# Optimization experiments

Measured on AMD Instinct MI355X. Metric: run time of the kernel, lower is better.

The kernel has to match this reference:

```python
import jax, jax.numpy as jnp
import numpy as np

B, N, F_IN, F_HID, F_OUT = 64, 1024, 64, 128, 64

def setup_inputs() -> dict:
    key = jax.random.key(0)
    ks = jax.random.split(key, 6)
    x = jax.random.normal(ks[0], (B, N, F_IN), dtype=jnp.float32)
    adj = jax.random.uniform(ks[1], (B, N, N), dtype=jnp.float32)
    mask = jax.random.randint(ks[2], (B, N), 0, 2).astype(bool)
    W1 = jax.random.normal(ks[3], (F_IN, F_HID), dtype=jnp.float32) * (1.0 / np.sqrt(F_IN))
    b1 = jnp.zeros((F_HID,), dtype=jnp.float32)
    W2 = jax.random.normal(ks[4], (F_HID, F_OUT), dtype=jnp.float32) * (1.0 / np.sqrt(F_HID))
    b2 = jnp.zeros((F_OUT,), dtype=jnp.float32)
    eps = jnp.zeros((1,), dtype=jnp.float32)
    return {"x": x, "adj": adj, "mask": mask, "W1": W1, "b1": b1, "W2": W2, "b2": b2, "eps": eps}

def reference(x, adj, mask, W1, b1, W2, b2, eps):
    # neighbor aggregation: out[b,i,f] = sum_j adj[b,i,j] * x[b,j,f]
    agg = jnp.einsum('bij,bjf->bif', adj, x)
    # add_loop=True: (1 + eps) * x + aggregated neighbors
    h = (1.0 + eps[0]) * x + agg
    # 2-layer GIN MLP applied per node (only valid nodes contribute in the
    # torch version via gather/scatter; invalid positions are zeroed)
    h = jax.nn.relu(h @ W1 + b1) @ W2 + b2
    return jnp.where(mask[..., None], h, jnp.zeros((), dtype=h.dtype))
```

## Files before the change

kernel.cpp:

```cpp
#include <hip/hip_runtime.h>


#define N_    1024
#define FIN   64
#define FHID  128
#define FOUT  64
#define JT    64
#define AS_LD 68
#define H1_LD 132

__global__ __launch_bounds__(256) void gin_fused(
    const float* __restrict__ x, const float* __restrict__ adj,
    const int* __restrict__ mask, const float* __restrict__ W1,
    const float* __restrict__ b1, const float* __restrict__ W2,
    const float* __restrict__ b2, const float* __restrict__ epsp,
    float* __restrict__ out)
{
    __shared__ float region1[8448];
    __shared__ float hs[64 * 64];

    float* xs  = region1;
    float* as_ = region1 + 4096;
    float* h1s = region1;

    const int t  = threadIdx.x;
    const int b  = blockIdx.x >> 4;
    const int i0 = (blockIdx.x & 15) * 64;

    const int fi = (t & 15) * 4;
    const int ri = (t >> 4) * 4;

    const float* xb   = x   + (size_t)b * N_ * FIN;
    const float* adjb = adj + (size_t)b * N_ * N_ + (size_t)i0 * N_;

    float4 acc[4];
    #pragma unroll
    for (int ii = 0; ii < 4; ++ii) acc[ii] = make_float4(0.f, 0.f, 0.f, 0.f);

    for (int jc = 0; jc < N_ / JT; ++jc) {
        const int j0 = jc * JT;

        const float4* xsrc = reinterpret_cast<const float4*>(xb + j0 * FIN);
        #pragma unroll
        for (int k = 0; k < 4; ++k) {
            const int l = t + 256 * k;
            reinterpret_cast<float4*>(xs)[l] = xsrc[l];
        }
        #pragma unroll
        for (int k = 0; k < 4; ++k) {
            const int l  = t + 256 * k;
            const int r  = l >> 4;
            const int c4 = (l & 15) * 4;
            const float4 v = *reinterpret_cast<const float4*>(adjb + (size_t)r * N_ + j0 + c4);
            *reinterpret_cast<float4*>(&as_[r * AS_LD + c4]) = v;
        }
        __syncthreads();

        #pragma unroll 4
        for (int jj = 0; jj < JT; ++jj) {
            const float4 xv = *reinterpret_cast<const float4*>(&xs[jj * FIN + fi]);
            const float a0 = as_[(ri + 0) * AS_LD + jj];
            const float a1 = as_[(ri + 1) * AS_LD + jj];
            const float a2 = as_[(ri + 2) * AS_LD + jj];
            const float a3 = as_[(ri + 3) * AS_LD + jj];
            acc[0].x += a0 * xv.x; acc[0].y += a0 * xv.y; acc[0].z += a0 * xv.z; acc[0].w += a0 * xv.w;
            acc[1].x += a1 * xv.x; acc[1].y += a1 * xv.y; acc[1].z += a1 * xv.z; acc[1].w += a1 * xv.w;
            acc[2].x += a2 * xv.x; acc[2].y += a2 * xv.y; acc[2].z += a2 * xv.z; acc[2].w += a2 * xv.w;
            acc[3].x += a3 * xv.x; acc[3].y += a3 * xv.y; acc[3].z += a3 * xv.z; acc[3].w += a3 * xv.w;
        }
        __syncthreads();
    }

    const float se = 1.0f + epsp[0];
    #pragma unroll
    for (int ii = 0; ii < 4; ++ii) {
        const float4 xv = *reinterpret_cast<const float4*>(xb + (size_t)(i0 + ri + ii) * FIN + fi);
        float4 h;
        h.x = acc[ii].x + se * xv.x;
        h.y = acc[ii].y + se * xv.y;
        h.z = acc[ii].z + se * xv.z;
        h.w = acc[ii].w + se * xv.w;
        *reinterpret_cast<float4*>(&hs[(ri + ii) * FIN + fi]) = h;
    }
    __syncthreads();

    {
        const int k4 = (t & 31) * 4;
        const int rb = (t >> 5) * 8;
        float4 hacc[8];
        const float4 b1v = *reinterpret_cast<const float4*>(b1 + k4);
        #pragma unroll
        for (int r = 0; r < 8; ++r) hacc[r] = b1v;

        #pragma unroll 4
        for (int j = 0; j < FIN; ++j) {
            const float4 w1v = *reinterpret_cast<const float4*>(W1 + j * FHID + k4);
            #pragma unroll
            for (int r = 0; r < 8; ++r) {
                const float hv = hs[(rb + r) * FIN + j];
                hacc[r].x += hv * w1v.x; hacc[r].y += hv * w1v.y;
                hacc[r].z += hv * w1v.z; hacc[r].w += hv * w1v.w;
            }
        }
        #pragma unroll
        for (int r = 0; r < 8; ++r) {
            float4 v;
            v.x = fmaxf(hacc[r].x, 0.f); v.y = fmaxf(hacc[r].y, 0.f);
            v.z = fmaxf(hacc[r].z, 0.f); v.w = fmaxf(hacc[r].w, 0.f);
            *reinterpret_cast<float4*>(&h1s[(rb + r) * H1_LD + k4]) = v;
        }
    }
    __syncthreads();

    {
        float4 oacc[4];
        const float4 b2v = *reinterpret_cast<const float4*>(b2 + fi);
        #pragma unroll
        for (int ii = 0; ii < 4; ++ii) oacc[ii] = b2v;

        #pragma unroll 4
        for (int j = 0; j < FHID; ++j) {
            const float4 w2v = *reinterpret_cast<const float4*>(W2 + j * FOUT + fi);
            #pragma unroll
            for (int ii = 0; ii < 4; ++ii) {
                const float hv = h1s[(ri + ii) * H1_LD + j];
                oacc[ii].x += hv * w2v.x; oacc[ii].y += hv * w2v.y;
                oacc[ii].z += hv * w2v.z; oacc[ii].w += hv * w2v.w;
            }
        }
        #pragma unroll
        for (int ii = 0; ii < 4; ++ii) {
            const int gi = i0 + ri + ii;
            const int m  = mask[b * N_ + gi];
            float4 o = oacc[ii];
            if (!m) o = make_float4(0.f, 0.f, 0.f, 0.f);
            *reinterpret_cast<float4*>(out + ((size_t)b * N_ + gi) * FOUT + fi) = o;
        }
    }
}

extern "C" void kernel_launch(void* const* d_in, const int* in_sizes, int n_in,
                              void* d_out, int out_size, void* d_ws, size_t ws_size,
                              hipStream_t stream) {
    const float* x    = (const float*)d_in[0];
    const float* adj  = (const float*)d_in[1];
    const int*   mask = (const int*)  d_in[2];
    const float* W1   = (const float*)d_in[3];
    const float* b1   = (const float*)d_in[4];
    const float* W2   = (const float*)d_in[5];
    const float* b2   = (const float*)d_in[6];
    const float* eps  = (const float*)d_in[7];
    float* out = (float*)d_out;

    dim3 grid(64 * 16);
    dim3 block(256);
    gin_fused<<<grid, block, 0, stream>>>(x, adj, mask, W1, b1, W2, b2, eps, out);
}
```

Before: 465.4 us.

## Use bf16 MFMA for adjacency aggregation with transposed bf16 LDS tiles

Replaces the scalar FP32 FMA loop for the adj·x aggregation with 32x32x16 bf16 MFMA instructions. Each 64x64 tile of adj and x is converted to bf16 on load and stored in LDS, with x transposed so both operands are K-contiguous. This targets the FP32 ALU-bound inner loop and halves LDS footprint. The cost is lower precision from rounding adj and x (1024-term sums) to bf16, plus extra conversion work and strided scalar loads of x.

```diff
diff --git a/kernel.cpp b/kernel.cpp
--- a/kernel.cpp
+++ b/kernel.cpp
@@ -5,9 +5,18 @@
 #define FIN   64
 #define FHID  128
 #define FOUT  64
-#define JT    64
-#define AS_LD 68
+#define HS_LD 68
 #define H1_LD 132
+#define FROW  9
+
+typedef __attribute__((ext_vector_type(16))) float f32x16;
+typedef __attribute__((ext_vector_type(8)))  short s16x8;
+
+__device__ inline short f2bf(float f) {
+    union { float f; unsigned int u; } v; v.f = f;
+    unsigned int r = v.u + 0x7fffu + ((v.u >> 16) & 1u);
+    return (short)(r >> 16);
+}
 
 __global__ __launch_bounds__(256) void gin_fused(
     const float* __restrict__ x, const float* __restrict__ adj,
@@ -16,71 +25,83 @@
     const float* __restrict__ b2, const float* __restrict__ epsp,
     float* __restrict__ out)
 {
-    __shared__ float region1[8448];
-    __shared__ float hs[64 * 64];
+    __shared__ s16x8 region1[2112];
+    __shared__ float hs[64 * HS_LD];
 
-    float* xs  = region1;
-    float* as_ = region1 + 4096;
-    float* h1s = region1;
+    s16x8 (*asf)[FROW] = reinterpret_cast<s16x8 (*)[FROW]>(region1);
+    s16x8 (*xtf)[FROW] = reinterpret_cast<s16x8 (*)[FROW]>(region1 + 576);
+    float* h1s = reinterpret_cast<float*>(region1);
 
-    const int t  = threadIdx.x;
-    const int b  = blockIdx.x >> 4;
-    const int i0 = (blockIdx.x & 15) * 64;
-
-    const int fi = (t & 15) * 4;
-    const int ri = (t >> 4) * 4;
+    const int t    = threadIdx.x;
+    const int lane = t & 63;
+    const int w    = t >> 6;
+    const int b    = blockIdx.x >> 4;
+    const int i0   = (blockIdx.x & 15) * 64;
 
     const float* xb   = x   + (size_t)b * N_ * FIN;
     const float* adjb = adj + (size_t)b * N_ * N_ + (size_t)i0 * N_;
 
-    float4 acc[4];
+    const int l31  = lane & 31;
+    const int half = lane >> 5;
+    const int mrow = (w & 1) * 32;
+    const int ncol = (w >> 1) * 32;
+
+    const int sr = t >> 2;
+    const int sc = (t & 3) * 16;
+    const int sg = (t & 3) * 2;
+
+    f32x16 acc;
     #pragma unroll
-    for (int ii = 0; ii < 4; ++ii) acc[ii] = make_float4(0.f, 0.f, 0.f, 0.f);
+    for (int r = 0; r < 16; ++r) acc[r] = 0.f;
 
-    for (int jc = 0; jc < N_ / JT; ++jc) {
-        const int j0 = jc * JT;
+    for (int jc = 0; jc < N_ / 64; ++jc) {
+        const int j0 = jc * 64;
 
-        const float4* xsrc = reinterpret_cast<const float4*>(xb + j0 * FIN);
-        #pragma unroll
-        for (int k = 0; k < 4; ++k) {
-            const int l = t + 256 * k;
-            reinterpret_cast<float4*>(xs)[l] = xsrc[l];
+        {
+            const float* ar = adjb + (size_t)sr * N_ + j0 + sc;
+            const float4 p0 = *reinterpret_cast<const float4*>(ar);
+            const float4 p1 = *reinterpret_cast<const float4*>(ar + 4);
+            const float4 p2 = *reinterpret_cast<const float4*>(ar + 8);
+            const float4 p3 = *reinterpret_cast<const float4*>(ar + 12);
+            s16x8 f0, f1;
+            f0[0] = f2bf(p0.x); f0[1] = f2bf(p0.y); f0[2] = f2bf(p0.z); f0[3] = f2bf(p0.w);
+            f0[4] = f2bf(p1.x); f0[5] = f2bf(p1.y); f0[6] = f2bf(p1.z); f0[7] = f2bf(p1.w);
+            f1[0] = f2bf(p2.x); f1[1] = f2bf(p2.y); f1[2] = f2bf(p2.z); f1[3] = f2bf(p2.w);
+            f1[4] = f2bf(p3.x); f1[5] = f2bf(p3.y); f1[6] = f2bf(p3.z); f1[7] = f2bf(p3.w);
+            asf[sr][sg]     = f0;
+            asf[sr][sg + 1] = f1;
         }
-        #pragma unroll
-        for (int k = 0; k < 4; ++k) {
-            const int l  = t + 256 * k;
-            const int r  = l >> 4;
-            const int c4 = (l & 15) * 4;
-            const float4 v = *reinterpret_cast<const float4*>(adjb + (size_t)r * N_ + j0 + c4);
-            *reinterpret_cast<float4*>(&as_[r * AS_LD + c4]) = v;
+        {
+            s16x8 q0, q1;
+            #pragma unroll
+            for (int jj = 0; jj < 8; ++jj)
+                q0[jj] = f2bf(xb[(size_t)(j0 + w * 16 + jj) * FIN + lane]);
+            #pragma unroll
+            for (int jj = 0; jj < 8; ++jj)
+                q1[jj] = f2bf(xb[(size_t)(j0 + w * 16 + 8 + jj) * FIN + lane]);
+            xtf[lane][2 * w]     = q0;
+            xtf[lane][2 * w + 1] = q1;
         }
         __syncthreads();
 
-        #pragma unroll 4
-        for (int jj = 0; jj < JT; ++jj) {
-            const float4 xv = *reinterpret_cast<const float4*>(&xs[jj * FIN + fi]);
-            const float a0 = as_[(ri + 0) * AS_LD + jj];
-            const float a1 = as_[(ri + 1) * AS_LD + jj];
-            const float a2 = as_[(ri + 2) * AS_LD + jj];
-            const float a3 = as_[(ri + 3) * AS_LD + jj];
-            acc[0].x += a0 * xv.x; acc[0].y += a0 * xv.y; acc[0].z += a0 * xv.z; acc[0].w += a0 * xv.w;
-            acc[1].x += a1 * xv.x; acc[1].y += a1 * xv.y; acc[1].z += a1 * xv.z; acc[1].w += a1 * xv.w;
-            acc[2].x += a2 * xv.x; acc[2].y += a2 * xv.y; acc[2].z += a2 * xv.z; acc[2].w += a2 * xv.w;
-            acc[3].x += a3 * xv.x; acc[3].y += a3 * xv.y; acc[3].z += a3 * xv.z; acc[3].w += a3 * xv.w;
+        #pragma unroll
+        for (int s = 0; s < 4; ++s) {
+            const s16x8 a  = asf[mrow + l31][2 * s + half];
+            const s16x8 bf = xtf[ncol + l31][2 * s + half];
+            acc = __builtin_amdgcn_mfma_f32_32x32x16_bf16(a, bf, acc, 0, 0, 0);
         }
         __syncthreads();
     }
 
-    const float se = 1.0f + epsp[0];
-    #pragma unroll
-    for (int ii = 0; ii < 4; ++ii) {
-        const float4 xv = *reinterpret_cast<const float4*>(xb + (size_t)(i0 + ri + ii) * FIN + fi);
-        float4 h;
-        h.x = acc[ii].x + se * xv.x;
-        h.y = acc[ii].y + se * xv.y;
-        h.z = acc[ii].z + se * xv.z;
-        h.w = acc[ii].w + se * xv.w;
-        *reinterpret_cast<float4*>(&hs[(ri + ii) * FIN + fi]) = h;
+    {
+        const float se = 1.0f + epsp[0];
+        const int col = ncol + l31;
+        #pragma unroll
+        for (int reg = 0; reg < 16; ++reg) {
+            const int row = mrow + (reg & 3) + 8 * (reg >> 2) + 4 * half;
+            const float xv = xb[(size_t)(i0 + row) * FIN + col];
+            hs[row * HS_LD + col] = acc[reg] + se * xv;
+        }
     }
     __syncthreads();
 
@@ -97,7 +118,7 @@
             const float4 w1v = *reinterpret_cast<const float4*>(W1 + j * FHID + k4);
             #pragma unroll
             for (int r = 0; r < 8; ++r) {
-                const float hv = hs[(rb + r) * FIN + j];
+                const float hv = hs[(rb + r) * HS_LD + j];
                 hacc[r].x += hv * w1v.x; hacc[r].y += hv * w1v.y;
                 hacc[r].z += hv * w1v.z; hacc[r].w += hv * w1v.w;
             }
@@ -113,6 +134,8 @@
     __syncthreads();
 
     {
+        const int fi = (t & 15) * 4;
+        const int ri = (t >> 4) * 4;
         float4 oacc[4];
         const float4 b2v = *reinterpret_cast<const float4*>(b2 + fi);
         #pragma unroll
```

Result: faster. 428.4 us (-8.0%).
